# Kernel optimization log

Hardware: AMD Instinct MI355X
Metric: run time of the kernel (lower is better)

## Reference

```python
import jax, jax.numpy as jnp
import numpy as np
from jax import lax

# Architecture constants (match init_kwargs)
B = 4          # clips
T_SEG = 8      # num_segments
D_IN = 256
D_HID = 64
H = 112
W = 112
WIN_T = 5      # window[0], temporal
WIN_S = 9      # window[1] == window[2], spatial
MAXD = WIN_S // 2


def setup_inputs() -> dict:
    key = jax.random.key(0)
    k1, k2, k3, k4 = jax.random.split(key, 4)
    x = jax.random.normal(k1, (B * T_SEG, D_IN, H, W), jnp.float32)
    conv_w = jax.random.normal(k2, (D_HID, D_IN, 3, 3), jnp.float32) * 0.05
    bn_gamma = jnp.ones((D_HID,), jnp.float32)
    bn_beta = jnp.zeros((D_HID,), jnp.float32)
    bn_mean = jax.random.normal(k3, (D_HID,), jnp.float32) * 0.1
    bn_var = jax.random.uniform(k4, (D_HID,), jnp.float32, minval=0.5, maxval=1.5)
    return {"x": x, "conv_w": conv_w, "bn_gamma": bn_gamma, "bn_beta": bn_beta,
            "bn_mean": bn_mean, "bn_var": bn_var}


def reference(x, conv_w, bn_gamma, bn_beta, bn_mean, bn_var):
    # downsample: Conv2d(k=3, s=2, p=1, no bias) + BatchNorm2d (eval) + ReLU
    y = lax.conv_general_dilated(x, conv_w, window_strides=(2, 2),
                                 padding=((1, 1), (1, 1)),
                                 dimension_numbers=("NCHW", "OIHW", "NCHW"))
    scale = bn_gamma / jnp.sqrt(bn_var + 1e-5)
    y = jax.nn.relu((y - bn_mean[:, None, None]) * scale[:, None, None]
                    + bn_beta[:, None, None])
    bt, c, h, w = y.shape
    b = bt // T_SEG
    y = y.reshape(b, T_SEG, c, h, w)
    # per-frame, per-pixel L2 normalization over channels (eps=1e-6, as in _L2normalize)
    yn = y / jnp.sqrt(jnp.sum(y * y, axis=2, keepdims=True) + 1e-6)
    # temporal zero-pad (padded frames normalize to 0 in the original too: 0/sqrt(eps)=0)
    half_t = WIN_T // 2
    ypad = jnp.pad(yn, ((0, 0), (half_t, half_t), (0, 0), (0, 0), (0, 0)))
    # spatial zero-pad by max displacement
    ypad = jnp.pad(ypad, ((0, 0), (0, 0), (0, 0), (MAXD, MAXD), (MAXD, MAXD)))
    # temporal windows: f2[b, t, l] = padded frame t+l   -> (b, T, L, c, h+2m, w+2m)
    f2 = jnp.stack([ypad[:, l:l + T_SEG] for l in range(WIN_T)], axis=2)
    # local windowed correlation (equivalent to einsum + _corr_abs_to_rel):
    # out[b,t,l,u,v,h,w] = sum_c yn[b,t,c,h,w] * f2[b,t,l,c,h+u,w+v]
    corrs = []
    for u in range(WIN_S):
        for v in range(WIN_S):
            corrs.append(jnp.einsum("btchw,btlchw->btlhw",
                                     yn, f2[:, :, :, :, u:u + h, v:v + w]))
    corr = jnp.stack(corrs, axis=-1).reshape(b, T_SEG, WIN_T, h, w, WIN_S, WIN_S)
    # '(b t l) u v h w -> b t h w 1 l u v'
    corr = jnp.transpose(corr, (0, 1, 3, 4, 2, 5, 6))
    return corr[:, :, :, :, None, :, :, :]
```

## Files before the change

### kernel.cpp

```cpp
#include <hip/hip_runtime.h>
#include <hip/hip_bf16.h>

#define TSEG 8
#define NBC 4
#define NBT 32
#define CIN 256
#define CH 64
#define HIN 112
#define WIN_ 112
#define HO 56
#define WO 56
#define HPD 64
#define WPD 64

#define FRSZE ((size_t)(HPD * WPD * CH))
#define ZF_U   147456
#define FR_U   (ZF_U + 262144)
#define WS_TOTAL_BYTES ((size_t)(FR_U + 32 * 262144) * 2)

typedef __attribute__((ext_vector_type(8))) short bf16x8;
typedef __attribute__((ext_vector_type(4))) float f32x4;

__device__ __forceinline__ unsigned short f2bf(float f) {
    union { float f; unsigned u; } c; c.f = f;
    unsigned u = c.u + 0x7fffu + ((c.u >> 16) & 1u);
    return (unsigned short)(u >> 16);
}

__global__ __launch_bounds__(256) void wprep_k(
    const float* __restrict__ w, unsigned short* __restrict__ wpp)
{
    int e = blockIdx.x * 256 + threadIdx.x;
    int cout = e / 2304;
    int rem  = e - cout * 2304;
    int ci   = rem / 9;
    int tap  = rem - ci * 9;
    wpp[((size_t)tap * 64 + cout) * 256 + ci] = f2bf(w[e]);
}

__global__ __launch_bounds__(256) void conv_mfma_k(
    const float* __restrict__ x, const unsigned short* __restrict__ wpp,
    const float* __restrict__ gamma, const float* __restrict__ beta,
    const float* __restrict__ mean, const float* __restrict__ var,
    unsigned short* __restrict__ frames)
{
    __shared__ unsigned short in_lds[5 * 120 * 32];
    __shared__ float sq[2][2][64];

    const int tid  = threadIdx.x;
    const int lane = tid & 63;
    const int wv   = tid >> 6;
    const int r    = wv >> 1;
    const int nh   = wv & 1;
    const int l15  = lane & 15;
    const int l4   = lane >> 4;

    const int bid = blockIdx.x + 28 * blockIdx.y;
    const int L   = (bid & 7) * 112 + (bid >> 3);
    const int hb  = L % 28;
    const int bt  = L / 28;

    const float* xb = x + (size_t)bt * (CIN * HIN * WIN_);

    f32x4 acc[4][2];
#pragma unroll
    for (int mt = 0; mt < 4; ++mt) {
        acc[mt][0] = (f32x4){0.f, 0.f, 0.f, 0.f};
        acc[mt][1] = (f32x4){0.f, 0.f, 0.f, 0.f};
    }

    int a_off[4][3];
#pragma unroll
    for (int mt = 0; mt < 4; ++mt) {
        int c = mt * 16 + l15; if (c > 55) c = 55;
#pragma unroll
        for (int kw = 0; kw < 3; ++kw) {
            int col = 2 * c + kw;
            int ba  = col * 64 + l4 * 16;
            ba ^= ((col >> 1) & 7) << 4;
            a_off[mt][kw] = ba;
        }
    }

    const unsigned short* bptr0 = wpp + ((size_t)(nh * 32 + l15) * 256 + l4 * 8);
    const unsigned short* bptr1 = wpp + ((size_t)(nh * 32 + 16 + l15) * 256 + l4 * 8);

    const int ih0 = 4 * hb - 1;

    for (int cb = 0; cb < 8; ++cb) {
        __syncthreads();
#pragma unroll
        for (int j = 0; j < 5; ++j) {
            const int jj  = wv + j * 4;
            const int row = jj >> 2, cig = jj & 3;
            const int ih  = ih0 + row;
            const int ihc = ih < 0 ? 0 : (ih > 111 ? 111 : ih);
            const float* xr = xb + ((size_t)(cb * 32 + cig * 8) * HIN + ihc) * WIN_;
            const bool rowin = (ih >= 0) && (ih < HIN);
#pragma unroll
            for (int p = 0; p < 2; ++p) {
                const int col = lane + p * 64;
                if (col < 113) {
                    const int iw  = col - 1;
                    const int iwc = iw < 0 ? 0 : iw;
                    const bool inb = rowin && (iw >= 0);
                    unsigned pk[4];
#pragma unroll
                    for (int q = 0; q < 4; ++q) {
                        float v0 = xr[(size_t)(2 * q) * HIN * WIN_ + iwc];
                        float v1 = xr[(size_t)(2 * q + 1) * HIN * WIN_ + iwc];
                        v0 = inb ? v0 : 0.f;
                        v1 = inb ? v1 : 0.f;
                        union { float f; unsigned u; } c0, c1; c0.f = v0; c1.f = v1;
                        unsigned u0 = c0.u + 0x7fffu + ((c0.u >> 16) & 1u);
                        unsigned u1 = c1.u + 0x7fffu + ((c1.u >> 16) & 1u);
                        pk[q] = (u0 >> 16) | (u1 & 0xffff0000u);
                    }
                    int ba = (row * 120 + col) * 64 + cig * 16;
                    ba ^= ((col >> 1) & 7) << 4;
                    *(uint4*)((char*)in_lds + ba) = make_uint4(pk[0], pk[1], pk[2], pk[3]);
                }
            }
        }
        __syncthreads();

        const int rowb = (2 * r) * 7680;
#pragma unroll
        for (int kh = 0; kh < 3; ++kh) {
            const int rb = rowb + kh * 7680;
#pragma unroll
            for (int kw = 0; kw < 3; ++kw) {
                const int tap = kh * 3 + kw;
                const bf16x8 bf0 = *(const bf16x8*)(bptr0 + tap * 16384 + cb * 32);
                const bf16x8 bf1 = *(const bf16x8*)(bptr1 + tap * 16384 + cb * 32);
#pragma unroll
                for (int mt = 0; mt < 4; ++mt) {
                    const bf16x8 af = *(const bf16x8*)((const char*)in_lds + (rb + a_off[mt][kw]));
                    acc[mt][0] = __builtin_amdgcn_mfma_f32_16x16x32_bf16(af, bf0, acc[mt][0], 0, 0, 0);
                    acc[mt][1] = __builtin_amdgcn_mfma_f32_16x16x32_bf16(af, bf1, acc[mt][1], 0, 0, 0);
                }
            }
        }
    }

    const int cout0 = nh * 32 + l15;
    const int cout1 = cout0 + 16;
    const float sc0 = gamma[cout0] * rsqrtf(var[cout0] + 1e-5f);
    const float bb0 = beta[cout0] - mean[cout0] * sc0;
    const float sc1 = gamma[cout1] * rsqrtf(var[cout1] + 1e-5f);
    const float bb1 = beta[cout1] - mean[cout1] * sc1;

    float yv[4][2][4];
    float ssr[4][4];
#pragma unroll
    for (int mt = 0; mt < 4; ++mt) {
#pragma unroll
        for (int reg = 0; reg < 4; ++reg) {
            float y0 = fmaxf(fmaf(acc[mt][0][reg], sc0, bb0), 0.f);
            float y1 = fmaxf(fmaf(acc[mt][1][reg], sc1, bb1), 0.f);
            yv[mt][0][reg] = y0; yv[mt][1][reg] = y1;
            float ss = y0 * y0 + y1 * y1;
            ss += __shfl_xor(ss, 1);
            ss += __shfl_xor(ss, 2);
            ss += __shfl_xor(ss, 4);
            ss += __shfl_xor(ss, 8);
            ssr[mt][reg] = ss;
        }
    }
    if (l15 == 0) {
#pragma unroll
        for (int mt = 0; mt < 4; ++mt)
#pragma unroll
            for (int reg = 0; reg < 4; ++reg)
                sq[r][nh][mt * 16 + l4 * 4 + reg] = ssr[mt][reg];
    }
    __syncthreads();

    const int h = 2 * hb + r;
    unsigned short* fdst = frames + (size_t)bt * FRSZE + (size_t)(h + 4) * WPD * CH;
#pragma unroll
    for (int mt = 0; mt < 4; ++mt) {
#pragma unroll
        for (int reg = 0; reg < 4; ++reg) {
            const int c = mt * 16 + l4 * 4 + reg;
            if (c < 56) {
                const float tot = sq[r][0][c] + sq[r][1][c];
                const float inv = rsqrtf(tot + 1e-6f);
                unsigned short* dp = fdst + (size_t)(c + 4) * CH;
                dp[cout0] = f2bf(yv[mt][0][reg] * inv);
                dp[cout1] = f2bf(yv[mt][1][reg] * inv);
            }
        }
    }
}

__global__ __launch_bounds__(64) void corr_mfma_k(
    const unsigned short* __restrict__ frames, float* __restrict__ out)
{
    __shared__ float so[2 * 56 * 84];

    const int lane = threadIdx.x;
    const int l15  = lane & 15;
    const int l4   = lane >> 4;

    const int bid = blockIdx.x;
    const int L   = (bid & 7) * 560 + (bid >> 3);
    const int hp  = L % 28;
    const int rem = L / 28;
    const int tl  = rem % 40;
    const int b   = rem / 40;
    const int t   = tl / 5, l = tl - 5 * t;
    const int h0  = hp * 2;
    const int bt  = b * TSEG + t;

    float* ob0 = out + (size_t)(bt * HO + h0) * (WO * 405) + l * 81;

    const int f = t + l;
    if (f < 2 || f > 9) {
#pragma unroll
        for (int hh = 0; hh < 2; ++hh) {
            float* ob = ob0 + (size_t)hh * (WO * 405);
#pragma unroll 4
            for (int w = 0; w < 56; ++w) {
                float* orow = ob + (size_t)w * 405;
                orow[lane] = 0.f;
                if (lane < 17) orow[lane + 64] = 0.f;
            }
        }
        return;
    }

    bf16x8 af[2][4][2];
#pragma unroll
    for (int hh = 0; hh < 2; ++hh) {
        const unsigned short* yrow = frames + (size_t)bt * FRSZE
                                   + (size_t)(h0 + hh + 4) * (WPD * CH);
#pragma unroll
        for (int m = 0; m < 4; ++m) {
            int w = (m << 4) + l15; if (w > 55) w = 55;
            const unsigned short* ap = yrow + (size_t)(w + 4) * CH + (l4 << 3);
            af[hh][m][0] = *(const bf16x8*)(ap);
            af[hh][m][1] = *(const bf16x8*)(ap + 32);
        }
    }

    const unsigned short* zb = frames + (size_t)(b * TSEG + f - 2) * FRSZE
                             + (size_t)h0 * (WPD * CH);

    const int PM[7] = {0, 0, 1, 1, 2, 2, 3};
    const int PN[7] = {0, 1, 1, 2, 2, 3, 3};

#define LOADB(buf, rr) { \
    const unsigned short* zr = zb + (size_t)(rr) * (WPD * CH); \
    _Pragma("unroll") \
    for (int n = 0; n < 4; ++n) { \
        const unsigned short* bp = zr + (size_t)((n << 4) + l15) * CH + (l4 << 3); \
        buf[n][0] = *(const bf16x8*)(bp); \
        buf[n][1] = *(const bf16x8*)(bp + 32); } }

#define COMPU(buf, hh, uu) { \
    f32x4 acc[7]; \
    _Pragma("unroll") \
    for (int i = 0; i < 7; ++i) acc[i] = (f32x4){0.f, 0.f, 0.f, 0.f}; \
    _Pragma("unroll") \
    for (int i = 0; i < 7; ++i) { \
        acc[i] = __builtin_amdgcn_mfma_f32_16x16x32_bf16(af[hh][PM[i]][0], buf[PN[i]][0], acc[i], 0, 0, 0); \
        acc[i] = __builtin_amdgcn_mfma_f32_16x16x32_bf16(af[hh][PM[i]][1], buf[PN[i]][1], acc[i], 0, 0, 0); } \
    _Pragma("unroll") \
    for (int i = 0; i < 7; ++i) { \
        const int zc = (PN[i] << 4) + l15; \
        const int w0 = (PM[i] << 4) + (l4 << 2); \
        _Pragma("unroll") \
        for (int rr2 = 0; rr2 < 4; ++rr2) { \
            const int w = w0 + rr2; \
            const int v = zc - w; \
            if (w < 56 && (unsigned)v <= 8u) \
                so[(hh) * 4704 + w * 84 + (uu) * 9 + v] = acc[i][rr2]; } } }

    bf16x8 b0[4][2], b1[4][2], b2[4][2];
    LOADB(b0, 0); LOADB(b1, 1); LOADB(b2, 2);
    COMPU(b0, 0, 0);                    LOADB(b0, 3);
    COMPU(b1, 0, 1); COMPU(b1, 1, 0);   LOADB(b1, 4);
    COMPU(b2, 0, 2); COMPU(b2, 1, 1);   LOADB(b2, 5);
    COMPU(b0, 0, 3); COMPU(b0, 1, 2);   LOADB(b0, 6);
    COMPU(b1, 0, 4); COMPU(b1, 1, 3);   LOADB(b1, 7);
    COMPU(b2, 0, 5); COMPU(b2, 1, 4);   LOADB(b2, 8);
    COMPU(b0, 0, 6); COMPU(b0, 1, 5);   LOADB(b0, 9);
    COMPU(b1, 0, 7); COMPU(b1, 1, 6);
    COMPU(b2, 0, 8); COMPU(b2, 1, 7);
    COMPU(b0, 1, 8);

#undef LOADB
#undef COMPU

#pragma unroll
    for (int hh = 0; hh < 2; ++hh) {
        float* ob = ob0 + (size_t)hh * (WO * 405);
        const float* sb = so + hh * 4704;
#pragma unroll 4
        for (int w = 0; w < 56; ++w) {
            const float* sr = sb + w * 84;
            float* orow = ob + (size_t)w * 405;
            orow[lane] = sr[lane];
            if (lane < 17) orow[lane + 64] = sr[lane + 64];
        }
    }
}

extern "C" void kernel_launch(void* const* d_in, const int* in_sizes, int n_in,
                              void* d_out, int out_size, void* d_ws, size_t ws_size,
                              hipStream_t stream)
{
    const float* x     = (const float*)d_in[0];
    const float* wgt   = (const float*)d_in[1];
    const float* gamma = (const float*)d_in[2];
    const float* beta  = (const float*)d_in[3];
    const float* mean  = (const float*)d_in[4];
    const float* var   = (const float*)d_in[5];
    float* out = (float*)d_out;

    unsigned short* wpp    = (unsigned short*)d_ws;
    unsigned short* frames = wpp + FR_U;

    if (ws_size < WS_TOTAL_BYTES) return;

    hipMemsetAsync(d_ws, 0, WS_TOTAL_BYTES, stream);
    wprep_k<<<dim3(576), 256, 0, stream>>>(wgt, wpp);
    conv_mfma_k<<<dim3(28, NBT), 256, 0, stream>>>(x, wpp, gamma, beta, mean, var, frames);
    corr_mfma_k<<<dim3(4480), 64, 0, stream>>>(frames, out);
}
```

Measured before the change: 291.8 us.

## Stream correlation output per displacement row and drop block-index swizzles

The correlation kernel no longer collects the full 2x56x81 tile in LDS and writes it out at the end. Each (hh,u) slab is staged through a small LDS buffer and written to global memory right after its MFMAs. This cuts LDS use per block, which may raise occupancy, but each write is only 9 floats per output row, so store coalescing gets worse. Both the conv and corr kernels also drop the XCD-aware block-index swizzle in favour of direct 2D/3D grid indexing, which changes L2 locality across chiplets.

```diff
diff --git a/kernel.cpp b/kernel.cpp
--- a/kernel.cpp
+++ b/kernel.cpp
@@ -54,11 +54,8 @@
     const int nh   = wv & 1;
     const int l15  = lane & 15;
     const int l4   = lane >> 4;
-
-    const int bid = blockIdx.x + 28 * blockIdx.y;
-    const int L   = (bid & 7) * 112 + (bid >> 3);
-    const int hb  = L % 28;
-    const int bt  = L / 28;
+    const int hb   = blockIdx.x;
+    const int bt   = blockIdx.y;
 
     const float* xb = x + (size_t)bt * (CIN * HIN * WIN_);
 
@@ -194,21 +191,21 @@
     }
 }
 
-__global__ __launch_bounds__(64) void corr_mfma_k(
+#define SSTR 12
+__global__ __launch_bounds__(64) void corr_pair_k(
     const unsigned short* __restrict__ frames, float* __restrict__ out)
 {
-    __shared__ float so[2 * 56 * 84];
+    __shared__ float so[2][56 * SSTR];
 
     const int lane = threadIdx.x;
     const int l15  = lane & 15;
     const int l4   = lane >> 4;
-
-    const int bid = blockIdx.x;
-    const int L   = (bid & 7) * 560 + (bid >> 3);
-    const int hp  = L % 28;
-    const int rem = L / 28;
-    const int tl  = rem % 40;
-    const int b   = rem / 40;
+    const int w7   = lane / 9;
+    const int v9   = lane - w7 * 9;
+
+    const int hp  = blockIdx.x;
+    const int tl  = blockIdx.y;
+    const int b   = blockIdx.z;
     const int t   = tl / 5, l = tl - 5 * t;
     const int h0  = hp * 2;
     const int bt  = b * TSEG + t;
@@ -258,7 +255,7 @@
         buf[n][0] = *(const bf16x8*)(bp); \
         buf[n][1] = *(const bf16x8*)(bp + 32); } }
 
-#define COMPU(buf, hh, uu) { \
+#define CS(buf, hh, uu) { \
     f32x4 acc[7]; \
     _Pragma("unroll") \
     for (int i = 0; i < 7; ++i) acc[i] = (f32x4){0.f, 0.f, 0.f, 0.f}; \
@@ -275,36 +272,31 @@
             const int w = w0 + rr2; \
             const int v = zc - w; \
             if (w < 56 && (unsigned)v <= 8u) \
-                so[(hh) * 4704 + w * 84 + (uu) * 9 + v] = acc[i][rr2]; } } }
+                so[hh][w * SSTR + v] = acc[i][rr2]; } } \
+    { \
+        float* obh = ob0 + (size_t)(hh) * (WO * 405) + (uu) * 9; \
+        _Pragma("unroll") \
+        for (int wb = 0; wb < 8; ++wb) { \
+            const int w = wb * 7 + w7; \
+            if (w < 56) obh[(size_t)w * 405 + v9] = so[hh][w * SSTR + v9]; \
+        } \
+    } }
 
     bf16x8 b0[4][2], b1[4][2], b2[4][2];
     LOADB(b0, 0); LOADB(b1, 1); LOADB(b2, 2);
-    COMPU(b0, 0, 0);                    LOADB(b0, 3);
-    COMPU(b1, 0, 1); COMPU(b1, 1, 0);   LOADB(b1, 4);
-    COMPU(b2, 0, 2); COMPU(b2, 1, 1);   LOADB(b2, 5);
-    COMPU(b0, 0, 3); COMPU(b0, 1, 2);   LOADB(b0, 6);
-    COMPU(b1, 0, 4); COMPU(b1, 1, 3);   LOADB(b1, 7);
-    COMPU(b2, 0, 5); COMPU(b2, 1, 4);   LOADB(b2, 8);
-    COMPU(b0, 0, 6); COMPU(b0, 1, 5);   LOADB(b0, 9);
-    COMPU(b1, 0, 7); COMPU(b1, 1, 6);
-    COMPU(b2, 0, 8); COMPU(b2, 1, 7);
-    COMPU(b0, 1, 8);
-
+    CS(b0, 0, 0);                    LOADB(b0, 3);
+    CS(b1, 0, 1); CS(b1, 1, 0);      LOADB(b1, 4);
+    CS(b2, 0, 2); CS(b2, 1, 1);      LOADB(b2, 5);
+    CS(b0, 0, 3); CS(b0, 1, 2);      LOADB(b0, 6);
+    CS(b1, 0, 4); CS(b1, 1, 3);      LOADB(b1, 7);
+    CS(b2, 0, 5); CS(b2, 1, 4);      LOADB(b2, 8);
+    CS(b0, 0, 6); CS(b0, 1, 5);      LOADB(b0, 9);
+    CS(b1, 0, 7); CS(b1, 1, 6);
+    CS(b2, 0, 8); CS(b2, 1, 7);
+    CS(b0, 1, 8);
+
+#undef CS
 #undef LOADB
-#undef COMPU
-
-#pragma unroll
-    for (int hh = 0; hh < 2; ++hh) {
-        float* ob = ob0 + (size_t)hh * (WO * 405);
-        const float* sb = so + hh * 4704;
-#pragma unroll 4
-        for (int w = 0; w < 56; ++w) {
-            const float* sr = sb + w * 84;
-            float* orow = ob + (size_t)w * 405;
-            orow[lane] = sr[lane];
-            if (lane < 17) orow[lane + 64] = sr[lane + 64];
-        }
-    }
 }
 
 extern "C" void kernel_launch(void* const* d_in, const int* in_sizes, int n_in,
@@ -327,5 +319,5 @@
     hipMemsetAsync(d_ws, 0, WS_TOTAL_BYTES, stream);
     wprep_k<<<dim3(576), 256, 0, stream>>>(wgt, wpp);
     conv_mfma_k<<<dim3(28, NBT), 256, 0, stream>>>(x, wpp, gamma, beta, mean, var, frames);
-    corr_mfma_k<<<dim3(4480), 64, 0, stream>>>(frames, out);
-}
+    corr_pair_k<<<dim3(28, 40, NBC), 64, 0, stream>>>(frames, out);
+}
```

After: 300.1 us. +2.8%, slower.
